# Optimization experiments

Measured on AMD Instinct MI355X. Metric: run time of the kernel, lower is better.

The kernel has to match this reference:

```python
import jax, jax.numpy as jnp
import numpy as np

B, S, D, H, M = 2, 2048, 1024, 16, 4096
DH = D // H
EPS = 1e-6  # flax LayerNorm default
THETA = 10000.0


def layer_norm(x, scale, bias):
    m = jnp.mean(x, axis=-1, keepdims=True)
    v = jnp.var(x, axis=-1, keepdims=True)
    return (x - m) * jax.lax.rsqrt(v + EPS) * scale + bias


def apply_rope(xq, xk):
    # xq, xk: [B, S, H, DH]; rotate consecutive pairs as complex numbers
    half = DH // 2
    freqs = 1.0 / THETA ** (jnp.arange(0, DH, 2)[:half].astype(jnp.float32) / DH)
    t = jnp.arange(S, dtype=jnp.float32)
    ang = jnp.outer(t, freqs)                      # [S, half]
    cos = jnp.cos(ang)[None, :, None, :]           # [1, S, 1, half]
    sin = jnp.sin(ang)[None, :, None, :]

    def rot(x):
        xr = x.astype(jnp.float32).reshape(*x.shape[:-1], half, 2)
        a, b = xr[..., 0], xr[..., 1]
        out = jnp.stack((a * cos - b * sin, a * sin + b * cos), axis=-1)
        return out.reshape(*x.shape).astype(jnp.float32)

    return rot(xq), rot(xk)


def setup_inputs() -> dict:
    key = jax.random.key(0)
    ks = jax.random.split(key, 12)
    sd = 1.0 / np.sqrt(D)
    return {
        "x": jax.random.normal(ks[0], (B, S, D), jnp.float32),
        "ln1_s": jnp.ones((D,), jnp.float32),
        "ln1_b": jnp.zeros((D,), jnp.float32),
        "wk": jax.random.normal(ks[1], (D, D), jnp.float32) * sd,
        "wq": jax.random.normal(ks[2], (D, D), jnp.float32) * sd,
        "wv": jax.random.normal(ks[3], (D, D), jnp.float32) * sd,
        "wo": jax.random.normal(ks[4], (D, D), jnp.float32) * sd,
        "ln2_s": jnp.ones((D,), jnp.float32),
        "ln2_b": jnp.zeros((D,), jnp.float32),
        "w1": jax.random.normal(ks[5], (D, M), jnp.float32) * sd,
        "b1": jnp.zeros((M,), jnp.float32),
        "w2": jax.random.normal(ks[6], (M, D), jnp.float32) * (1.0 / np.sqrt(M)),
        "b2": jnp.zeros((D,), jnp.float32),
    }


def reference(x, ln1_s, ln1_b, wk, wq, wv, wo, ln2_s, ln2_b, w1, b1, w2, b2):
    h = layer_norm(x, ln1_s, ln1_b)
    xk = (h @ wk).reshape(B, S, H, DH)
    xq = (h @ wq).reshape(B, S, H, DH)
    xv = (h @ wv).reshape(B, S, H, DH)
    xq, xk = apply_rope(xq, xk)
    # scores: [B, H, S, S]
    scores = jnp.einsum("bqhd,bkhd->bhqk", xq, xk) / jnp.sqrt(jnp.float32(DH))
    attn = jax.nn.softmax(scores, axis=-1)
    ctx = jnp.einsum("bhqk,bkhd->bqhd", attn, xv).reshape(B, S, D)
    attn_out = ctx @ wo
    mlp_in = attn_out + x
    h2 = layer_norm(mlp_in, ln2_s, ln2_b)
    h2 = jax.nn.gelu(h2 @ w1 + b1)  # approximate gelu (jax default, matches source)
    h2 = h2 @ w2 + b2
    return h2 + mlp_in
```

## Files before the change

kernel.cpp:

```cpp
#include <hip/hip_runtime.h>
#include <stdint.h>

#define B_ 2
#define S_ 2048
#define D_ 1024
#define H_ 16
#define DH_ 64
#define M_ 4096
#define BS_ 4096

typedef __attribute__((ext_vector_type(8))) short short8;
typedef __attribute__((ext_vector_type(4))) float f32x4;
typedef __attribute__((ext_vector_type(16))) float f32x16;

static __device__ __forceinline__ unsigned short f2bf(float f) {
  unsigned u = __float_as_uint(f);
  u += 0x7fffu + ((u >> 16) & 1u);
  return (unsigned short)(u >> 16);
}
static __device__ __forceinline__ float bf2f(unsigned short s) {
  return __uint_as_float(((unsigned)s) << 16);
}
static __device__ __forceinline__ f32x4 MFMA16(short8 a, short8 b, f32x4 c) {
  return __builtin_amdgcn_mfma_f32_16x16x32_bf16(a, b, c, 0, 0, 0);
}
static __device__ __forceinline__ f32x16 MFMA32(short8 a, short8 b, f32x16 c) {
  return __builtin_amdgcn_mfma_f32_32x32x16_bf16(a, b, c, 0, 0, 0);
}
static __device__ __forceinline__ void gload_lds16(const void* g, void* l) {
  __builtin_amdgcn_global_load_lds(
      (const __attribute__((address_space(1))) unsigned int*)g,
      (__attribute__((address_space(3))) unsigned int*)l, 16, 0, 0);
}
static __device__ __forceinline__ unsigned cvtpk_bf16(float lo, float hi) {
  unsigned r;
  asm("v_cvt_pk_bf16_f32 %0, %1, %2" : "=v"(r) : "v"(lo), "v"(hi));
  return r;
}
static __device__ __forceinline__ float gelu_f(float x) {
  float u = 0.7978845608028654f * (x + 0.044715f * x * x * x);
  return 0.5f * x * (1.0f + tanhf(u));
}

__global__ __launch_bounds__(256) void tcast_kernel(const float* __restrict__ in,
                                                    unsigned short* __restrict__ out,
                                                    int R, int C) {
  __shared__ float tile[32][33];
  int tx = threadIdx.x & 31, ty = threadIdx.x >> 5;
  int r0 = blockIdx.y * 32, c0 = blockIdx.x * 32;
#pragma unroll
  for (int i = 0; i < 4; ++i)
    tile[ty + i * 8][tx] = in[(size_t)(r0 + ty + i * 8) * C + c0 + tx];
  __syncthreads();
#pragma unroll
  for (int i = 0; i < 4; ++i)
    out[(size_t)(c0 + ty + i * 8) * R + r0 + tx] = f2bf(tile[tx][ty + i * 8]);
}

__global__ __launch_bounds__(256) void ln_kernel(const float* __restrict__ x,
                                                 const float* __restrict__ sc,
                                                 const float* __restrict__ bi,
                                                 unsigned short* __restrict__ out) {
  int row = blockIdx.x;
  int t = threadIdx.x;
  float4 v = ((const float4*)(x + (size_t)row * D_))[t];
  float s1 = v.x + v.y + v.z + v.w;
  float s2 = v.x * v.x + v.y * v.y + v.z * v.z + v.w * v.w;
#pragma unroll
  for (int m = 1; m < 64; m <<= 1) {
    s1 += __shfl_xor(s1, m);
    s2 += __shfl_xor(s2, m);
  }
  __shared__ float red[8];
  int w = t >> 6, l = t & 63;
  if (l == 0) { red[w] = s1; red[4 + w] = s2; }
  __syncthreads();
  s1 = red[0] + red[1] + red[2] + red[3];
  s2 = red[4] + red[5] + red[6] + red[7];
  float mean = s1 * (1.0f / D_);
  float var = s2 * (1.0f / D_) - mean * mean;
  float rstd = rsqrtf(var + 1e-6f);
  float4 scv = ((const float4*)sc)[t];
  float4 biv = ((const float4*)bi)[t];
  ushort4 o;
  o.x = f2bf((v.x - mean) * rstd * scv.x + biv.x);
  o.y = f2bf((v.y - mean) * rstd * scv.y + biv.y);
  o.z = f2bf((v.z - mean) * rstd * scv.z + biv.z);
  o.w = f2bf((v.w - mean) * rstd * scv.w + biv.w);
  ((ushort4*)out)[(size_t)row * (D_ / 4) + t] = o;
}

__global__ __launch_bounds__(256) void rope_kernel(unsigned short* __restrict__ t_,
                                                   float qscale) {
  size_t idx = (size_t)blockIdx.x * 256 + threadIdx.x;
  int c = (int)(idx & 7);
  size_t rowi = idx >> 3;
  int s = (int)(rowi & (S_ - 1));
  unsigned short* p = t_ + rowi * DH_ + c * 8;
  short8 v = *(const short8*)p;
  unsigned short o[8];
#pragma unroll
  for (int i = 0; i < 4; ++i) {
    int pi = c * 4 + i;
    float freq = exp2f(-(float)pi * 0.4152410118609203f);
    float ang = (float)s * freq;
    float sn, cs;
    sincosf(ang, &sn, &cs);
    float a = bf2f((unsigned short)v[2 * i]);
    float b = bf2f((unsigned short)v[2 * i + 1]);
    o[2 * i] = f2bf((a * cs - b * sn) * qscale);
    o[2 * i + 1] = f2bf((a * sn + b * cs) * qscale);
  }
  short8 ov;
#pragma unroll
  for (int i = 0; i < 8; ++i) ov[i] = (short)o[i];
  *(short8*)p = ov;
}

__global__ __launch_bounds__(256) void attn_kernel(const unsigned short* __restrict__ q,
                                                   const unsigned short* __restrict__ k,
                                                   const unsigned short* __restrict__ vt,
                                                   unsigned short* __restrict__ ctx) {
  __shared__ char smem[49152];
  const int tid = threadIdx.x, w = tid >> 6, l = tid & 63;
  const int lo = l & 31, hi = l >> 5;
  char* Ps = smem + 32768 + w * 4096;
  int flat = blockIdx.y * 16 + blockIdx.x;
  int swz = (flat & 7) * 64 + (flat >> 3);
  const int bh = swz >> 4;
  const int b = bh >> 4, h = bh & 15;
  const int q0 = (swz & 15) * 128 + w * 32;

  const unsigned short* qbase = q + ((size_t)bh * S_ + q0 + lo) * DH_ + hi * 8;
  short8 qf[4];
#pragma unroll
  for (int c = 0; c < 4; ++c) qf[c] = *(const short8*)(qbase + c * 16);

  const unsigned short* kb = k + (size_t)bh * S_ * DH_;
  const unsigned short* vb = vt + (size_t)bh * DH_ * S_;

  short8 onesB;
#pragma unroll
  for (int i = 0; i < 8; ++i) onesB[i] = (short)0x3F80;

  f32x16 o0, o1, lac;
#pragma unroll
  for (int i = 0; i < 16; ++i) { o0[i] = 0.f; o1[i] = 0.f; lac[i] = 0.f; }

#define STAGE_KV(buf, kt)                                                        \
  {                                                                              \
    char* Ks_ = smem + (buf) * 16384;                                            \
    char* Vs_ = Ks_ + 8192;                                                      \
    _Pragma("unroll") for (int i = 0; i < 2; ++i) {                              \
      int slot = i * 256 + tid;                                                  \
      int r = slot >> 3, pc = slot & 7;                                          \
      int sc_ = pc ^ (r & 7);                                                    \
      gload_lds16(kb + (size_t)((kt) + r) * DH_ + sc_ * 8,                       \
                  Ks_ + (i * 4096 + w * 1024));                                  \
      gload_lds16(vb + (size_t)r * S_ + (kt) + sc_ * 8,                          \
                  Vs_ + (i * 4096 + w * 1024));                                  \
    }                                                                            \
  }

  STAGE_KV(0, 0);
  asm volatile("s_waitcnt vmcnt(0)" ::: "memory");
  __builtin_amdgcn_s_barrier();

  for (int t = 0; t < S_ / 64; ++t) {
    int buf = t & 1;
    if (t + 1 < S_ / 64) STAGE_KV(buf ^ 1, (t + 1) * 64);
    char* Ks = smem + buf * 16384;
    char* Vs = Ks + 8192;

#pragma unroll
    for (int kt2 = 0; kt2 < 2; ++kt2) {
      f32x16 z;
#pragma unroll
      for (int i = 0; i < 16; ++i) z[i] = 0.f;
      __builtin_amdgcn_s_setprio(1);
#pragma unroll
      for (int c = 0; c < 4; ++c) {
        int r = kt2 * 32 + lo;
        short8 kf = *(const short8*)(Ks + r * 128 + (((hi + 2 * c) ^ (r & 7)) << 4));
        z = MFMA32(kf, qf[c], z);
      }
      __builtin_amdgcn_s_setprio(0);
      unsigned pk[8];
#pragma unroll
      for (int e = 0; e < 8; ++e)
        pk[e] = cvtpk_bf16(exp2f(z[2 * e]), exp2f(z[2 * e + 1]));
#pragma unroll
      for (int s2 = 0; s2 < 4; ++s2) {
        uint2 dd;
        dd.x = pk[2 * s2];
        dd.y = pk[2 * s2 + 1];
        int slot = kt2 * 4 + s2;
        *(uint2*)(Ps + lo * 128 + ((slot ^ (lo & 7)) << 4) + hi * 8) = dd;
      }
    }

    __builtin_amdgcn_s_setprio(1);
#pragma unroll
    for (int c = 0; c < 4; ++c) {
      short8 pa = *(const short8*)(Ps + lo * 128 + (((2 * c + hi) ^ (lo & 7)) << 4));
      lac = MFMA32(pa, onesB, lac);
      int r0v = lo, r1v = 32 + lo;
      short8 vf0 = *(const short8*)(Vs + r0v * 128 + (((2 * c + hi) ^ (r0v & 7)) << 4));
      short8 vf1 = *(const short8*)(Vs + r1v * 128 + (((2 * c + hi) ^ (r1v & 7)) << 4));
      o0 = MFMA32(pa, vf0, o0);
      o1 = MFMA32(pa, vf1, o1);
    }
    __builtin_amdgcn_s_setprio(0);
    asm volatile("s_waitcnt vmcnt(0)" ::: "memory");
    __builtin_amdgcn_s_barrier();
  }

#pragma unroll
  for (int r = 0; r < 16; ++r) {
    float rl = 1.0f / lac[r];
    int srow = q0 + (r & 3) + 8 * (r >> 2) + 4 * hi;
    unsigned short* cp = ctx + ((size_t)(b * S_) + srow) * D_ + h * DH_ + lo;
    cp[0] = f2bf(o0[r] * rl);
    cp[32] = f2bf(o1[r] * rl);
  }
#undef STAGE_KV
}

template <int EPI>
__global__ __launch_bounds__(256) void gemm_bt(const unsigned short* __restrict__ A,
                                               const unsigned short* __restrict__ Bt,
                                               int K,
                                               const float* __restrict__ aux0,
                                               const float* __restrict__ aux1,
                                               void* __restrict__ out0,
                                               void* __restrict__ out1,
                                               void* __restrict__ out2) {
  __shared__ char smem[65536];
  int tid = threadIdx.x, w = tid >> 6, l = tid & 63;
  int wr = w >> 1, wc = w & 1;
  int flat = blockIdx.y * gridDim.x + blockIdx.x;
  int xcd = flat & 7, j = flat >> 3;
  int row0 = (xcd * 4 + (j & 3)) * 128;
  int col0 = (j >> 2) * 128;
  f32x4 acc[4][4];
#pragma unroll
  for (int mt = 0; mt < 4; ++mt)
#pragma unroll
    for (int nt = 0; nt < 4; ++nt) {
      f32x4 z = {0.f, 0.f, 0.f, 0.f};
      acc[mt][nt] = z;
    }
  int lr = l >> 3, lc = l & 7;

#define STAGE_AB(base, kt)                                                       \
  {                                                                              \
    char* As_ = smem + (base);                                                   \
    char* Bs_ = As_ + 16384;                                                     \
    _Pragma("unroll") for (int i = 0; i < 4; ++i) {                              \
      int rb = w * 32 + i * 8;                                                   \
      int r = rb + lr;                                                           \
      int sc_ = lc ^ (r & 7);                                                    \
      gload_lds16(A + (size_t)(row0 + r) * K + (kt) + sc_ * 8, As_ + rb * 128);  \
      gload_lds16(Bt + (size_t)(col0 + r) * K + (kt) + sc_ * 8, Bs_ + rb * 128); \
    }                                                                            \
  }

#define COMPUTE_STEP(As, Bs)                                                     \
  {                                                                              \
    _Pragma("unroll") for (int kf = 0; kf < 2; ++kf) {                           \
      short8 af[4], bfr[4];                                                      \
      _Pragma("unroll") for (int mt = 0; mt < 4; ++mt) {                         \
        int r = wr * 64 + mt * 16 + (l & 15);                                    \
        int c = (l >> 4) + 4 * kf;                                               \
        af[mt] = *(const short8*)((As) + r * 128 + ((c ^ (r & 7)) << 4));        \
      }                                                                          \
      _Pragma("unroll") for (int nt = 0; nt < 4; ++nt) {                         \
        int r = wc * 64 + nt * 16 + (l & 15);                                    \
        int c = (l >> 4) + 4 * kf;                                               \
        bfr[nt] = *(const short8*)((Bs) + r * 128 + ((c ^ (r & 7)) << 4));       \
      }                                                                          \
      _Pragma("unroll") for (int mt = 0; mt < 4; ++mt)                           \
          _Pragma("unroll") for (int nt = 0; nt < 4; ++nt)                       \
              acc[mt][nt] = MFMA16(af[mt], bfr[nt], acc[mt][nt]);                \
    }                                                                            \
  }

  const int NT = K >> 6;
  STAGE_AB(0, 0);
  asm volatile("s_waitcnt vmcnt(0)" ::: "memory");
  __builtin_amdgcn_s_barrier();
  for (int t = 0; t < NT; ++t) {
    int buf = t & 1;
    if (t + 1 < NT) STAGE_AB((buf ^ 1) * 32768, (t + 1) * 64);
    char* As = smem + buf * 32768;
    COMPUTE_STEP(As, As + 16384);
    asm volatile("s_waitcnt vmcnt(0)" ::: "memory");
    __builtin_amdgcn_s_barrier();
  }
#undef STAGE_AB
#undef COMPUTE_STEP

#pragma unroll
  for (int mt = 0; mt < 4; ++mt) {
#pragma unroll
    for (int nt = 0; nt < 4; ++nt) {
      int grow0 = row0 + wr * 64 + mt * 16 + ((l >> 4) << 2);
      int gcol = col0 + wc * 64 + nt * 16 + (l & 15);
      if (EPI == 0) {
        int which = gcol >> 10;
        int d = gcol & 1023;
        int hh = d >> 6, dh = d & 63;
#pragma unroll
        for (int r = 0; r < 4; ++r) {
          int grow = grow0 + r;
          int b = grow >> 11, s = grow & 2047;
          float v = acc[mt][nt][r];
          if (which == 0)
            ((unsigned short*)out0)[(((size_t)(b * H_ + hh)) * S_ + s) * DH_ + dh] = f2bf(v);
          else if (which == 1)
            ((unsigned short*)out1)[(((size_t)(b * H_ + hh)) * S_ + s) * DH_ + dh] = f2bf(v);
          else
            ((unsigned short*)out2)[(((size_t)(b * H_ + hh)) * DH_ + dh) * S_ + s] = f2bf(v);
        }
      } else if (EPI == 1) {
        float* mo = (float*)out0;
#pragma unroll
        for (int r = 0; r < 4; ++r) {
          int grow = grow0 + r;
          mo[(size_t)grow * D_ + gcol] = acc[mt][nt][r] + aux0[(size_t)grow * D_ + gcol];
        }
      } else if (EPI == 2) {
        unsigned short* gq = (unsigned short*)out0;
        float bb = aux0[gcol];
#pragma unroll
        for (int r = 0; r < 4; ++r) {
          int grow = grow0 + r;
          gq[(size_t)grow * M_ + gcol] = f2bf(gelu_f(acc[mt][nt][r] + bb));
        }
      } else {
        float* po = (float*)out0;
        float bb = aux0[gcol];
#pragma unroll
        for (int r = 0; r < 4; ++r) {
          int grow = grow0 + r;
          po[(size_t)grow * D_ + gcol] =
              acc[mt][nt][r] + bb + aux1[(size_t)grow * D_ + gcol];
        }
      }
    }
  }
}

extern "C" void kernel_launch(void* const* d_in, const int* in_sizes, int n_in,
                              void* d_out, int out_size, void* d_ws, size_t ws_size,
                              hipStream_t stream) {
  const float* x = (const float*)d_in[0];
  const float* ln1s = (const float*)d_in[1];
  const float* ln1b = (const float*)d_in[2];
  const float* wk = (const float*)d_in[3];
  const float* wq = (const float*)d_in[4];
  const float* wv = (const float*)d_in[5];
  const float* wo = (const float*)d_in[6];
  const float* ln2s = (const float*)d_in[7];
  const float* ln2b = (const float*)d_in[8];
  const float* w1 = (const float*)d_in[9];
  const float* b1 = (const float*)d_in[10];
  const float* w2 = (const float*)d_in[11];
  const float* b2 = (const float*)d_in[12];

  char* ws = (char*)d_ws;
  unsigned short* wqkv_t = (unsigned short*)(ws);
  unsigned short* wo_t = (unsigned short*)(ws + 6291456);
  unsigned short* w1_t = (unsigned short*)(ws + 8388608);
  unsigned short* w2_t = (unsigned short*)(ws + 16777216);
  unsigned short* h_bf = (unsigned short*)(ws + 25165824);
  unsigned short* q_bf = (unsigned short*)(ws + 33554432);
  unsigned short* k_bf = (unsigned short*)(ws + 41943040);
  unsigned short* vt_bf = (unsigned short*)(ws + 50331648);
  unsigned short* ctx_bf = (unsigned short*)(ws + 58720256);
  float* mlp_in = (float*)(ws + 67108864);
  unsigned short* g_bf = (unsigned short*)(ws + 83886080);

  dim3 blk(256);
  tcast_kernel<<<dim3(32, 32), blk, 0, stream>>>(wq, wqkv_t, 1024, 1024);
  tcast_kernel<<<dim3(32, 32), blk, 0, stream>>>(wk, wqkv_t + 1048576, 1024, 1024);
  tcast_kernel<<<dim3(32, 32), blk, 0, stream>>>(wv, wqkv_t + 2097152, 1024, 1024);
  tcast_kernel<<<dim3(32, 32), blk, 0, stream>>>(wo, wo_t, 1024, 1024);
  tcast_kernel<<<dim3(128, 32), blk, 0, stream>>>(w1, w1_t, 1024, 4096);
  tcast_kernel<<<dim3(32, 128), blk, 0, stream>>>(w2, w2_t, 4096, 1024);
  ln_kernel<<<dim3(BS_), blk, 0, stream>>>(x, ln1s, ln1b, h_bf);
  gemm_bt<0><<<dim3(24, 32), blk, 0, stream>>>(h_bf, wqkv_t, 1024, nullptr, nullptr,
                                               q_bf, k_bf, vt_bf);
  rope_kernel<<<dim3(2048), blk, 0, stream>>>(q_bf, 0.125f * 1.4426950408889634f);
  rope_kernel<<<dim3(2048), blk, 0, stream>>>(k_bf, 1.0f);
  attn_kernel<<<dim3(16, 32), blk, 0, stream>>>(q_bf, k_bf, vt_bf, ctx_bf);
  gemm_bt<1><<<dim3(8, 32), blk, 0, stream>>>(ctx_bf, wo_t, 1024, x, nullptr,
                                              mlp_in, nullptr, nullptr);
  ln_kernel<<<dim3(BS_), blk, 0, stream>>>(mlp_in, ln2s, ln2b, h_bf);
  gemm_bt<2><<<dim3(32, 32), blk, 0, stream>>>(h_bf, w1_t, 1024, b1, nullptr,
                                               g_bf, nullptr, nullptr);
  gemm_bt<3><<<dim3(8, 32), blk, 0, stream>>>(g_bf, w2_t, 4096, b2, mlp_in,
                                              (float*)d_out, nullptr, nullptr);
}
```

Baseline: 373.8 us.

## Split attention over key halves with combine pass and add 256x256 GELU GEMM

Attention is now split into two key-range halves per query tile, doubling the grid to 1024 blocks. Each half writes unnormalized bf16 partial outputs and row sums into reused workspace, and a separate combine kernel sums and normalizes them. The aim is better CU occupancy, since the old 512-block launch underfilled the device. Separately, the FFN up-projection moves to a new 512-thread kernel with 256x256 tiles and 128KB of dynamic LDS, for more data reuse per block. The cost is extra memory traffic and a launch for the combine step, plus extra bf16 rounding of the partial outputs.

```diff
diff --git a/kernel.cpp b/kernel.cpp
--- a/kernel.cpp
+++ b/kernel.cpp
@@ -117,19 +117,25 @@
   *(short8*)p = ov;
 }
 
-__global__ __launch_bounds__(256) void attn_kernel(const unsigned short* __restrict__ q,
-                                                   const unsigned short* __restrict__ k,
-                                                   const unsigned short* __restrict__ vt,
-                                                   unsigned short* __restrict__ ctx) {
+__global__ __launch_bounds__(256) void attn_part_kernel(
+    const unsigned short* __restrict__ q, const unsigned short* __restrict__ k,
+    const unsigned short* __restrict__ vt, unsigned short* __restrict__ po,
+    float* __restrict__ pl) {
   __shared__ char smem[49152];
   const int tid = threadIdx.x, w = tid >> 6, l = tid & 63;
   const int lo = l & 31, hi = l >> 5;
   char* Ps = smem + 32768 + w * 4096;
-  int flat = blockIdx.y * 16 + blockIdx.x;
-  int swz = (flat & 7) * 64 + (flat >> 3);
-  const int bh = swz >> 4;
+  int flat = blockIdx.x;
+  int xcd = flat & 7, j = flat >> 3;
+  const int bh = xcd * 4 + (j >> 5);
+  int sub = j & 31;
+  const int qt = sub >> 1, ks = sub & 1;
   const int b = bh >> 4, h = bh & 15;
-  const int q0 = (swz & 15) * 128 + w * 32;
+  const int q0 = qt * 128 + w * 32;
+  const int kbase = ks * 1024;
+
+  unsigned short* po_k = po + (size_t)ks * (B_ * S_ * D_);
+  float* pl_k = pl + (size_t)ks * (32 * S_);
 
   const unsigned short* qbase = q + ((size_t)bh * S_ + q0 + lo) * DH_ + hi * 8;
   short8 qf[4];
@@ -162,13 +168,13 @@
     }                                                                            \
   }
 
-  STAGE_KV(0, 0);
+  STAGE_KV(0, kbase);
   asm volatile("s_waitcnt vmcnt(0)" ::: "memory");
   __builtin_amdgcn_s_barrier();
 
-  for (int t = 0; t < S_ / 64; ++t) {
+  for (int t = 0; t < 16; ++t) {
     int buf = t & 1;
-    if (t + 1 < S_ / 64) STAGE_KV(buf ^ 1, (t + 1) * 64);
+    if (t + 1 < 16) STAGE_KV(buf ^ 1, kbase + (t + 1) * 64);
     char* Ks = smem + buf * 16384;
     char* Vs = Ks + 8192;
 
@@ -217,13 +223,33 @@
 
 #pragma unroll
   for (int r = 0; r < 16; ++r) {
-    float rl = 1.0f / lac[r];
     int srow = q0 + (r & 3) + 8 * (r >> 2) + 4 * hi;
-    unsigned short* cp = ctx + ((size_t)(b * S_) + srow) * D_ + h * DH_ + lo;
-    cp[0] = f2bf(o0[r] * rl);
-    cp[32] = f2bf(o1[r] * rl);
+    unsigned short* cp = po_k + ((size_t)(b * S_) + srow) * D_ + h * DH_ + lo;
+    cp[0] = f2bf(o0[r]);
+    cp[32] = f2bf(o1[r]);
+    if (lo == 0) pl_k[(size_t)bh * S_ + srow] = lac[r];
   }
 #undef STAGE_KV
+}
+
+__global__ __launch_bounds__(256) void attn_combine_kernel(
+    const unsigned short* __restrict__ po, const float* __restrict__ pl,
+    unsigned short* __restrict__ ctx) {
+  size_t i8 = (size_t)blockIdx.x * 256 + threadIdx.x;
+  size_t i = i8 * 8;
+  int d = (int)(i & 1023);
+  int h = d >> 6;
+  int s = (int)((i >> 10) & 2047);
+  int b = (int)(i >> 21);
+  size_t lidx = ((size_t)(b * 16 + h)) * S_ + s;
+  float rl = 1.0f / (pl[lidx] + pl[(size_t)(32 * S_) + lidx]);
+  short8 a = *(const short8*)(po + i);
+  short8 c = *(const short8*)(po + (size_t)(B_ * S_ * D_) + i);
+  short8 o;
+#pragma unroll
+  for (int j = 0; j < 8; ++j)
+    o[j] = (short)f2bf((bf2f((unsigned short)a[j]) + bf2f((unsigned short)c[j])) * rl);
+  *(short8*)(ctx + i) = o;
 }
 
 template <int EPI>
@@ -329,14 +355,6 @@
           int grow = grow0 + r;
           mo[(size_t)grow * D_ + gcol] = acc[mt][nt][r] + aux0[(size_t)grow * D_ + gcol];
         }
-      } else if (EPI == 2) {
-        unsigned short* gq = (unsigned short*)out0;
-        float bb = aux0[gcol];
-#pragma unroll
-        for (int r = 0; r < 4; ++r) {
-          int grow = grow0 + r;
-          gq[(size_t)grow * M_ + gcol] = f2bf(gelu_f(acc[mt][nt][r] + bb));
-        }
       } else {
         float* po = (float*)out0;
         float bb = aux0[gcol];
@@ -346,6 +364,92 @@
           po[(size_t)grow * D_ + gcol] =
               acc[mt][nt][r] + bb + aux1[(size_t)grow * D_ + gcol];
         }
+      }
+    }
+  }
+}
+
+__global__ __launch_bounds__(512, 2) void gemm256_gelu(
+    const unsigned short* __restrict__ A, const unsigned short* __restrict__ Bt,
+    const float* __restrict__ bias, unsigned short* __restrict__ out) {
+  extern __shared__ char smem[];
+  const int K = 1024;
+  int tid = threadIdx.x, w = tid >> 6, l = tid & 63;
+  int wr = w >> 2, wc = w & 3;
+  int flat = blockIdx.y * gridDim.x + blockIdx.x;
+  int xcd = flat & 7, j = flat >> 3;
+  int row0 = (xcd * 2 + (j & 1)) * 256;
+  int col0 = (j >> 1) * 256;
+  f32x4 acc[8][4];
+#pragma unroll
+  for (int mt = 0; mt < 8; ++mt)
+#pragma unroll
+    for (int nt = 0; nt < 4; ++nt) {
+      f32x4 z = {0.f, 0.f, 0.f, 0.f};
+      acc[mt][nt] = z;
+    }
+  int lr = l >> 3, lc = l & 7;
+
+#define STAGE_AB(base, kt)                                                        \
+  {                                                                               \
+    char* As_ = smem + (base);                                                    \
+    char* Bs_ = As_ + 32768;                                                      \
+    _Pragma("unroll") for (int i = 0; i < 4; ++i) {                               \
+      int r = i * 64 + w * 8 + lr;                                                \
+      int sc_ = lc ^ (r & 7);                                                     \
+      gload_lds16(A + (size_t)(row0 + r) * K + (kt) + sc_ * 8,                    \
+                  As_ + (i * 8192 + w * 1024));                                   \
+      gload_lds16(Bt + (size_t)(col0 + r) * K + (kt) + sc_ * 8,                   \
+                  Bs_ + (i * 8192 + w * 1024));                                   \
+    }                                                                             \
+  }
+
+#define COMPUTE_STEP(As, Bs)                                                      \
+  {                                                                               \
+    _Pragma("unroll") for (int kf = 0; kf < 2; ++kf) {                            \
+      short8 af[8], bfr[4];                                                       \
+      _Pragma("unroll") for (int mt = 0; mt < 8; ++mt) {                          \
+        int r = wr * 128 + mt * 16 + (l & 15);                                    \
+        int c = (l >> 4) + 4 * kf;                                                \
+        af[mt] = *(const short8*)((As) + r * 128 + ((c ^ (r & 7)) << 4));         \
+      }                                                                           \
+      _Pragma("unroll") for (int nt = 0; nt < 4; ++nt) {                          \
+        int r = wc * 64 + nt * 16 + (l & 15);                                     \
+        int c = (l >> 4) + 4 * kf;                                                \
+        bfr[nt] = *(const short8*)((Bs) + r * 128 + ((c ^ (r & 7)) << 4));        \
+      }                                                                           \
+      _Pragma("unroll") for (int mt = 0; mt < 8; ++mt)                            \
+          _Pragma("unroll") for (int nt = 0; nt < 4; ++nt)                        \
+              acc[mt][nt] = MFMA16(af[mt], bfr[nt], acc[mt][nt]);                 \
+    }                                                                             \
+  }
+
+  const int NT = K >> 6;
+  STAGE_AB(0, 0);
+  asm volatile("s_waitcnt vmcnt(0)" ::: "memory");
+  __builtin_amdgcn_s_barrier();
+  for (int t = 0; t < NT; ++t) {
+    int buf = t & 1;
+    if (t + 1 < NT) STAGE_AB((buf ^ 1) * 65536, (t + 1) * 64);
+    char* As = smem + buf * 65536;
+    COMPUTE_STEP(As, As + 32768);
+    asm volatile("s_waitcnt vmcnt(0)" ::: "memory");
+    __builtin_amdgcn_s_barrier();
+  }
+#undef STAGE_AB
+#undef COMPUTE_STEP
+
+#pragma unroll
+  for (int mt = 0; mt < 8; ++mt) {
+#pragma unroll
+    for (int nt = 0; nt < 4; ++nt) {
+      int grow0 = row0 + wr * 128 + mt * 16 + ((l >> 4) << 2);
+      int gcol = col0 + wc * 64 + nt * 16 + (l & 15);
+      float bb = bias[gcol];
+#pragma unroll
+      for (int r = 0; r < 4; ++r) {
+        int grow = grow0 + r;
+        out[(size_t)grow * M_ + gcol] = f2bf(gelu_f(acc[mt][nt][r] + bb));
       }
     }
   }
@@ -381,6 +485,12 @@
   float* mlp_in = (float*)(ws + 67108864);
   unsigned short* g_bf = (unsigned short*)(ws + 83886080);
 
+  unsigned short* po = (unsigned short*)mlp_in;
+  float* pl = (float*)h_bf;
+
+  hipFuncSetAttribute((const void*)gemm256_gelu,
+                      hipFuncAttributeMaxDynamicSharedMemorySize, 131072);
+
   dim3 blk(256);
   tcast_kernel<<<dim3(32, 32), blk, 0, stream>>>(wq, wqkv_t, 1024, 1024);
   tcast_kernel<<<dim3(32, 32), blk, 0, stream>>>(wk, wqkv_t + 1048576, 1024, 1024);
@@ -393,12 +503,12 @@
                                                q_bf, k_bf, vt_bf);
   rope_kernel<<<dim3(2048), blk, 0, stream>>>(q_bf, 0.125f * 1.4426950408889634f);
   rope_kernel<<<dim3(2048), blk, 0, stream>>>(k_bf, 1.0f);
-  attn_kernel<<<dim3(16, 32), blk, 0, stream>>>(q_bf, k_bf, vt_bf, ctx_bf);
+  attn_part_kernel<<<dim3(1024), blk, 0, stream>>>(q_bf, k_bf, vt_bf, po, pl);
+  attn_combine_kernel<<<dim3(2048), blk, 0, stream>>>(po, pl, ctx_bf);
   gemm_bt<1><<<dim3(8, 32), blk, 0, stream>>>(ctx_bf, wo_t, 1024, x, nullptr,
                                               mlp_in, nullptr, nullptr);
   ln_kernel<<<dim3(BS_), blk, 0, stream>>>(mlp_in, ln2s, ln2b, h_bf);
-  gemm_bt<2><<<dim3(32, 32), blk, 0, stream>>>(h_bf, w1_t, 1024, b1, nullptr,
-                                               g_bf, nullptr, nullptr);
+  gemm256_gelu<<<dim3(16, 16), dim3(512), 131072, stream>>>(h_bf, w1_t, b1, g_bf);
   gemm_bt<3><<<dim3(8, 32), blk, 0, stream>>>(g_bf, w2_t, 4096, b2, mlp_in,
                                               (float*)d_out, nullptr, nullptr);
 }
```

Result: no change. 379.6 us (+1.6%).
